# Kernel tuning notes

Measured on AMD Instinct MI355X. Metric: run time of the kernel, lower is better.

The kernel has to match this reference:

```python
import jax, jax.numpy as jnp
import numpy as np

B, SQ, SK = 2, 2048, 2048   # batch, n_query, n_memory
D, H, DFF = 1024, 16, 1024  # model dim, heads, ffn dim (must equal D per source constraints)
DH = D // H                 # head dim = 64
NEG = 1e9


def _split_heads(x):
    # (B, S, D) -> (B, H, S, DH)
    b, s, _ = x.shape
    return x.reshape(b, s, H, DH).transpose(0, 2, 1, 3)


def setup_inputs() -> dict:
    key = jax.random.key(0)
    ks = jax.random.split(key, 10)
    s = 0.02
    return {
        "q": jax.random.normal(ks[0], (B, SQ, D), jnp.float32),
        "k": jax.random.normal(ks[1], (B, SK, D), jnp.float32),
        "v": jax.random.normal(ks[2], (B, SK, D), jnp.float32),
        "Win_w": jax.random.normal(ks[3], (DFF, D), jnp.float32) * s,
        "Win_b": jnp.zeros((DFF,), jnp.float32),
        "Wff_w": jax.random.normal(ks[4], (D, DFF), jnp.float32) * s,
        "Wff_b": jnp.zeros((D,), jnp.float32),
        "Wout_w": jax.random.normal(ks[5], (D, D), jnp.float32) * s,
        "Wout_b": jnp.zeros((D,), jnp.float32),
        "attn_mask": jax.random.randint(ks[6], (B, SK), 0, 2, jnp.int32),
    }


def reference(q, k, v, Win_w, Win_b, Wff_w, Wff_b, Wout_w, Wout_b, attn_mask):
    # projections (in_linear; k,v additionally pass through out_linear as in source)
    qh = q @ Win_w.T + Win_b
    kh = (k @ Win_w.T + Win_b) @ Wout_w.T + Wout_b
    vh = (v @ Win_w.T + Win_b) @ Wout_w.T + Wout_b
    qh = qh * (D ** -0.5)

    qh, kh, vh = _split_heads(qh), _split_heads(kh), _split_heads(vh)

    # additive mask bias: 0 where mask==1, -1e9 where mask==0, broadcast over heads/queries
    bias = (attn_mask.astype(jnp.float32) - 1.0) * NEG  # (B, SK)
    scores = jnp.einsum("bhqd,bhkd->bhqk", qh, kh) + bias[:, None, None, :]
    probs = jax.nn.softmax(scores, axis=-1)
    out = jnp.einsum("bhqk,bhkd->bhqd", probs, vh)

    # merge heads: (B, H, SQ, DH) -> (B, SQ, D)
    out = out.transpose(0, 2, 1, 3).reshape(B, SQ, D)

    out = out @ Wff_w.T + Wff_b
    out = out @ Wout_w.T + Wout_b
    return out
```

## Files before the change

### kernel.cpp

```cpp
#include <hip/hip_runtime.h>
#include <cstdint>
#include <cstddef>

using u16 = unsigned short;
using u32 = unsigned int;

typedef __attribute__((ext_vector_type(8))) short short8;
typedef __attribute__((ext_vector_type(4))) float f32x4;

#define MFMA16(a, b, c) __builtin_amdgcn_mfma_f32_16x16x32_bf16((a), (b), (c), 0, 0, 0)

#define QSCALE 0.0450842200f

__device__ __forceinline__ u16 f2bf(float f) {
  u32 u = __float_as_uint(f);
  return (u16)((u + 0x7FFFu + ((u >> 16) & 1u)) >> 16);
}

__device__ __forceinline__ u32 pack_bf16(float a, float b) {
  u32 r;
  asm("v_cvt_pk_bf16_f32 %0, %1, %2" : "=v"(r) : "v"(a), "v"(b));
  return r;
}

__device__ __forceinline__ void gload_lds16(const u16* g, u16* l) {
  __builtin_amdgcn_global_load_lds((const __attribute__((address_space(1))) void*)g,
                                   (__attribute__((address_space(3))) void*)l, 16, 0, 0);
}

__global__ __launch_bounds__(256) void cvt_qkv(const float* __restrict__ q,
                                               const float* __restrict__ k,
                                               const float* __restrict__ v,
                                               u16* __restrict__ X) {
  int i4 = blockIdx.x * 256 + threadIdx.x;
  const float* src = (i4 < 1048576) ? q : (i4 < 2097152) ? k : v;
  int loc = i4 & 1048575;
  float4 w = reinterpret_cast<const float4*>(src)[loc];
  u32 lo = (u32)f2bf(w.x) | ((u32)f2bf(w.y) << 16);
  u32 hi = (u32)f2bf(w.z) | ((u32)f2bf(w.w) << 16);
  reinterpret_cast<uint2*>(X)[i4] = make_uint2(lo, hi);
}

__global__ __launch_bounds__(256) void prep(const float* __restrict__ Wout_w,
                                            const float* __restrict__ Win_w,
                                            const float* __restrict__ Wff_w,
                                            const float* __restrict__ Win_b,
                                            u16* __restrict__ Woutb, u16* __restrict__ Winb,
                                            u16* __restrict__ WinT, u16* __restrict__ WffT,
                                            float* __restrict__ bias1f) {
  __shared__ float tile[64][68];
  const int t = threadIdx.x;
  const int bid = blockIdx.x;
  if (bid < 2048) {
    const float* src = bid < 1024 ? Wout_w : Win_w;
    u16* dst = bid < 1024 ? Woutb : Winb;
    const float sc = bid < 1024 ? 1.0f : QSCALE;
    int i = (bid & 1023) * 256 + t;
    float4 v = reinterpret_cast<const float4*>(src)[i];
    u32 lo = (u32)f2bf(v.x * sc) | ((u32)f2bf(v.y * sc) << 16);
    u32 hi = (u32)f2bf(v.z * sc) | ((u32)f2bf(v.w * sc) << 16);
    reinterpret_cast<uint2*>(dst)[i] = make_uint2(lo, hi);
  } else if (bid < 2560) {
    const float* in = bid < 2304 ? Win_w : Wff_w;
    u16* out = bid < 2304 ? WinT : WffT;
    const int tix = (bid - 2048) & 255;
    const int bx = (tix >> 4) * 64, by = (tix & 15) * 64;
    const int r = t >> 2, c16 = (t & 3) * 16;
#pragma unroll
    for (int i = 0; i < 4; ++i)
      *reinterpret_cast<float4*>(&tile[r][c16 + i * 4]) =
          *reinterpret_cast<const float4*>(&in[(size_t)(bx + r) * 1024 + by + c16 + i * 4]);
    __syncthreads();
    const int jj = t >> 2, i16 = (t & 3) * 16;
#pragma unroll
    for (int i = 0; i < 4; ++i) {
      uint2 p;
      p.x = (u32)f2bf(tile[i16 + i * 4 + 0][jj]) | ((u32)f2bf(tile[i16 + i * 4 + 1][jj]) << 16);
      p.y = (u32)f2bf(tile[i16 + i * 4 + 2][jj]) | ((u32)f2bf(tile[i16 + i * 4 + 3][jj]) << 16);
      *reinterpret_cast<uint2*>(&out[(size_t)(by + jj) * 1024 + bx + i16 + i * 4]) = p;
    }
  } else {
    float4 v = reinterpret_cast<const float4*>(Win_b)[t];
    v.x *= QSCALE; v.y *= QSCALE; v.z *= QSCALE; v.w *= QSCALE;
    reinterpret_cast<float4*>(bias1f)[t] = v;
  }
}

__global__ __launch_bounds__(256) void bias_comb(const float* __restrict__ W,
                                                 const float* __restrict__ bin,
                                                 const float* __restrict__ badd,
                                                 float* __restrict__ outb) {
  const int w = threadIdx.x >> 6, l = threadIdx.x & 63;
  const int j = blockIdx.x * 4 + w;
  const float4* Wr = reinterpret_cast<const float4*>(W + (size_t)j * 1024);
  const float4* br = reinterpret_cast<const float4*>(bin);
  float s = 0.f;
  for (int i = l; i < 256; i += 64) {
    float4 a = Wr[i], b = br[i];
    s += a.x * b.x + a.y * b.y + a.z * b.z + a.w * b.w;
  }
#pragma unroll
  for (int o = 1; o < 64; o <<= 1) s += __shfl_xor(s, o);
  if (l == 0) outb[j] = s + badd[j];
}

__global__ __launch_bounds__(256) void gemm_w2(const u16* __restrict__ A,
                                               const u16* __restrict__ Bt0,
                                               const u16* __restrict__ Bt1,
                                               u16* __restrict__ C0,
                                               u16* __restrict__ C1) {
  const u16* Bt = blockIdx.z ? Bt1 : Bt0;
  u16* C = blockIdx.z ? C1 : C0;
  __shared__ __align__(16) u16 As[2][4096];
  __shared__ __align__(16) u16 Bs[2][4096];
  const int t = threadIdx.x, w = t >> 6, l = t & 63;
  const int l15 = l & 15, l4 = l >> 4;
  const int m0 = blockIdx.x * 64, n0 = blockIdx.y * 64;
  f32x4 acc[4] = {};
  const int row0 = t >> 3, cs0 = t & 7;
  const int c0 = cs0 ^ (row0 & 7);
  const int row1 = row0 + 32;
  const int c1 = cs0 ^ (row1 & 7);
  const u16* gA0 = A + (size_t)(m0 + row0) * 1024 + c0 * 8;
  const u16* gA1 = A + (size_t)(m0 + row1) * 1024 + c1 * 8;
  const u16* gB0 = Bt + (size_t)(n0 + row0) * 1024 + c0 * 8;
  const u16* gB1 = Bt + (size_t)(n0 + row1) * 1024 + c1 * 8;
#define W2_STAGE(KK, DST)                             \
  gload_lds16(gA0 + (KK), &As[DST][0] + w * 512);     \
  gload_lds16(gA1 + (KK), &As[DST][2048] + w * 512);  \
  gload_lds16(gB0 + (KK), &Bs[DST][0] + w * 512);     \
  gload_lds16(gB1 + (KK), &Bs[DST][2048] + w * 512);
  W2_STAGE(0, 0)
  for (int step = 0; step < 16; ++step) {
    const int c = step & 1;
    __syncthreads();
    if (step < 15) { W2_STAGE((step + 1) * 64, c ^ 1) }
#pragma unroll
    for (int ks = 0; ks < 2; ++ks) {
      const int cc = ks * 4 + l4;
      short8 bfr = *reinterpret_cast<const short8*>(&Bs[c][(w * 16 + l15) * 64 + ((cc ^ (l15 & 7)) * 8)]);
#pragma unroll
      for (int i = 0; i < 4; ++i) {
        short8 afr = *reinterpret_cast<const short8*>(&As[c][(i * 16 + l15) * 64 + ((cc ^ (l15 & 7)) * 8)]);
        acc[i] = MFMA16(afr, bfr, acc[i]);
      }
    }
  }
#pragma unroll
  for (int i = 0; i < 4; ++i)
#pragma unroll
    for (int j = 0; j < 4; ++j)
      C[(size_t)(m0 + i * 16 + l4 * 4 + j) * 1024 + n0 + w * 16 + l15] = f2bf(acc[i][j]);
}

__global__ __launch_bounds__(256) void proj(const u16* __restrict__ X,
                                            const u16* __restrict__ Winb,
                                            const u16* __restrict__ Wc2,
                                            const float* __restrict__ bias1f,
                                            const float* __restrict__ bias2,
                                            u16* __restrict__ Qh,
                                            u16* __restrict__ Kp,
                                            u16* __restrict__ VT) {
  __shared__ __align__(16) u16 As[2][4096];
  __shared__ __align__(16) u16 Bs[2][4096];
  const int t = threadIdx.x, w = t >> 6, l = t & 63;
  const int l15 = l & 15, l4 = l >> 4;
  const int seg = blockIdx.x >> 5;
  const int m0 = blockIdx.x * 128;
  const int n0 = blockIdx.y * 128;
  const int wr = (w >> 1) * 64, wc = (w & 1) * 64;
  const u16* Bt = seg == 0 ? Winb : Wc2;
  const float* bias = seg == 0 ? bias1f : bias2;

  f32x4 acc[4][4] = {};
  const u16* gA = X + (size_t)(m0 + (t >> 2)) * 1024 + (t & 3) * 8;
  const u16* gB = Bt + (size_t)(n0 + (t >> 2)) * 1024 + (t & 3) * 8;
#define PJ_STAGE(KK, DST)                                   \
  gload_lds16(gA + (KK), &As[DST][0] + w * 512);            \
  gload_lds16(gA + (KK) + 65536, &As[DST][2048] + w * 512); \
  gload_lds16(gB + (KK), &Bs[DST][0] + w * 512);            \
  gload_lds16(gB + (KK) + 65536, &Bs[DST][2048] + w * 512);
  PJ_STAGE(0, 0)
  for (int step = 0; step < 32; ++step) {
    const int c = step & 1;
    __syncthreads();
    if (step < 31) { PJ_STAGE((step + 1) * 32, c ^ 1) }
    short8 af[4], bf[4];
#pragma unroll
    for (int i = 0; i < 4; ++i)
      af[i] = *reinterpret_cast<const short8*>(&As[c][(wr + i * 16 + l15) * 32 + l4 * 8]);
#pragma unroll
    for (int i = 0; i < 4; ++i)
      bf[i] = *reinterpret_cast<const short8*>(&Bs[c][(wc + i * 16 + l15) * 32 + l4 * 8]);
#pragma unroll
    for (int mi = 0; mi < 4; ++mi)
#pragma unroll
      for (int ni = 0; ni < 4; ++ni)
        acc[mi][ni] = MFMA16(af[mi], bf[ni], acc[mi][ni]);
  }

#pragma unroll
  for (int mi = 0; mi < 4; ++mi) {
#pragma unroll
    for (int ni = 0; ni < 4; ++ni) {
      const int col = n0 + wc + ni * 16 + l15;
      const float bv = bias[col];
      const int row0 = m0 + wr + mi * 16 + l4 * 4;
      if (seg == 0) {
#pragma unroll
        for (int j = 0; j < 4; ++j)
          Qh[(size_t)(row0 + j) * 1024 + col] = f2bf(acc[mi][ni][j] + bv);
      } else if (seg == 1) {
#pragma unroll
        for (int j = 0; j < 4; ++j)
          Kp[(size_t)(row0 - 4096 + j) * 1024 + col] = f2bf(acc[mi][ni][j] + bv);
      } else {
        const int r = row0 - 8192;
        const int bb = r >> 11;
        const int sk = r & 2047;
        u32 p0 = (u32)f2bf(acc[mi][ni][0] + bv) | ((u32)f2bf(acc[mi][ni][1] + bv) << 16);
        u32 p1 = (u32)f2bf(acc[mi][ni][2] + bv) | ((u32)f2bf(acc[mi][ni][3] + bv) << 16);
        *reinterpret_cast<uint2*>(VT + ((size_t)(bb * 1024 + col)) * 2048 + sk) = make_uint2(p0, p1);
      }
    }
  }
}

__global__ __launch_bounds__(512) void attn(const u16* __restrict__ Qh,
                                            const u16* __restrict__ Kb,
                                            const u16* __restrict__ VT,
                                            const int* __restrict__ mask,
                                            u16* __restrict__ AO) {
  __shared__ __align__(16) u16 Kt[64 * 64];
  __shared__ __align__(16) u16 Vt[64 * 64];
  __shared__ __align__(16) u16 Pw[8 * 16 * 64];
  __shared__ float biasS[2048];
  const int t = threadIdx.x, l = t & 63, w = t >> 6;
  const int l15 = l & 15, l4 = l >> 4;
  const int q0 = blockIdx.x * 128;
  const int bh = blockIdx.y, b = bh >> 4, h = bh & 15;

  for (int i = t; i < 2048; i += 512) biasS[i] = mask[b * 2048 + i] ? 0.f : -1.442695e9f;

  short8 qf[2];
  {
    const u16* qp = Qh + (size_t)(b * 2048 + q0 + w * 16 + l15) * 1024 + h * 64 + l4 * 8;
    qf[0] = *reinterpret_cast<const short8*>(qp);
    qf[1] = *reinterpret_cast<const short8*>(qp + 32);
  }
  short8 ones;
#pragma unroll
  for (int i = 0; i < 8; ++i) ones[i] = (short)0x3F80;

  f32x4 acc[4] = {};
  f32x4 accS = {};

  const int rr = t >> 3, cs = t & 7;
  const int ck = cs ^ (rr & 7);
  const u16* gK = Kb + (size_t)(b * 2048 + rr) * 1024 + h * 64 + ck * 8;
  u16* ldsK = Kt + w * 512;
  const u32* gV = reinterpret_cast<const u32*>(VT) + (size_t)(b * 1024 + h * 64 + rr) * 1024 + ck;
  const int pws = w * 1024;

  for (int kt = 0; kt < 2048; kt += 64) {
    const u32* gvt = gV + (kt >> 1);
    u32 A0 = gvt[0], A1 = gvt[8], A2 = gvt[16], A3 = gvt[24];
    __syncthreads();
    gload_lds16(gK + (size_t)kt * 1024, ldsK);
    uint4 vv;
    vv.x = (A0 & 0xffffu) | (A1 << 16);
    vv.y = (A2 & 0xffffu) | (A3 << 16);
    vv.z = (A0 >> 16) | (A1 & 0xffff0000u);
    vv.w = (A2 >> 16) | (A3 & 0xffff0000u);
    *reinterpret_cast<uint4*>(&Vt[rr * 64 + cs * 8]) = vv;
    __syncthreads();

    f32x4 s[4] = {};
#pragma unroll
    for (int ks = 0; ks < 2; ++ks) {
      const int cc = ks * 4 + l4;
#pragma unroll
      for (int n = 0; n < 4; ++n) {
        short8 kb = *reinterpret_cast<const short8*>(&Kt[(n * 16 + l15) * 64 + ((cc ^ (l15 & 7)) * 8)]);
        s[n] = MFMA16(qf[ks], kb, s[n]);
      }
    }
#pragma unroll
    for (int n = 0; n < 4; ++n) {
      const float bv = biasS[kt + n * 16 + l15];
#pragma unroll
      for (int j = 0; j < 4; ++j) s[n][j] = __builtin_amdgcn_exp2f(s[n][j] + bv);
    }
#pragma unroll
    for (int j = 0; j < 4; ++j) {
      const int r = l4 * 4 + j;
      uint2 pk;
      pk.x = pack_bf16(s[0][j], s[1][j]);
      pk.y = pack_bf16(s[2][j], s[3][j]);
      *reinterpret_cast<uint2*>(
          &Pw[pws + r * 64 + (((l15 >> 1) ^ (r & 7)) * 8) + (l15 & 1) * 4]) = pk;
    }
#pragma unroll
    for (int ks = 0; ks < 2; ++ks) {
      const int cc = ks * 4 + l4;
      short8 pa = *reinterpret_cast<const short8*>(&Pw[pws + l15 * 64 + ((cc ^ (l15 & 7)) * 8)]);
#pragma unroll
      for (int n = 0; n < 4; ++n) {
        short8 vb = *reinterpret_cast<const short8*>(&Vt[(n * 16 + l15) * 64 + ((cc ^ (l15 & 7)) * 8)]);
        acc[n] = MFMA16(pa, vb, acc[n]);
      }
      accS = MFMA16(pa, ones, accS);
    }
  }

  const size_t orow0 = (size_t)(b * 2048 + q0 + w * 16 + l4 * 4);
#pragma unroll
  for (int j = 0; j < 4; ++j) {
    const float inv = 1.0f / accS[j];
#pragma unroll
    for (int n = 0; n < 4; ++n)
      AO[(orow0 + j) * 1024 + h * 64 + n * 16 + l15] = f2bf(acc[n][j] * inv);
  }
}

__global__ __launch_bounds__(256) void gemm_tail(const u16* __restrict__ A,
                                                 const u16* __restrict__ Bt,
                                                 const float* __restrict__ bias,
                                                 float* __restrict__ C) {
  __shared__ __align__(16) u16 As[2][4096];
  __shared__ __align__(16) u16 Bs[2][2048];
  const int t = threadIdx.x, w = t >> 6, l = t & 63;
  const int l15 = l & 15, l4 = l >> 4;
  const int m0 = blockIdx.x * 128, n0 = blockIdx.y * 64;
  const int wr = (w >> 1) * 64, wc = (w & 1) * 32;
  f32x4 acc[4][2] = {};
  const u16* gA = A + (size_t)(m0 + (t >> 2)) * 1024 + (t & 3) * 8;
  const u16* gB = Bt + (size_t)(n0 + (t >> 2)) * 1024 + (t & 3) * 8;
#define TL_STAGE(KK, DST)                                   \
  gload_lds16(gA + (KK), &As[DST][0] + w * 512);            \
  gload_lds16(gA + (KK) + 65536, &As[DST][2048] + w * 512); \
  gload_lds16(gB + (KK), &Bs[DST][0] + w * 512);
  TL_STAGE(0, 0)
  for (int step = 0; step < 32; ++step) {
    const int c = step & 1;
    __syncthreads();
    if (step < 31) { TL_STAGE((step + 1) * 32, c ^ 1) }
    short8 af[4], bf[2];
#pragma unroll
    for (int i = 0; i < 4; ++i)
      af[i] = *reinterpret_cast<const short8*>(&As[c][(wr + i * 16 + l15) * 32 + l4 * 8]);
#pragma unroll
    for (int i = 0; i < 2; ++i)
      bf[i] = *reinterpret_cast<const short8*>(&Bs[c][(wc + i * 16 + l15) * 32 + l4 * 8]);
#pragma unroll
    for (int mi = 0; mi < 4; ++mi)
#pragma unroll
      for (int ni = 0; ni < 2; ++ni)
        acc[mi][ni] = MFMA16(af[mi], bf[ni], acc[mi][ni]);
  }
#pragma unroll
  for (int mi = 0; mi < 4; ++mi) {
#pragma unroll
    for (int ni = 0; ni < 2; ++ni) {
      const int col = n0 + wc + ni * 16 + l15;
      const float bv = bias[col];
      const int row0 = m0 + wr + mi * 16 + l4 * 4;
#pragma unroll
      for (int j = 0; j < 4; ++j)
        C[(size_t)(row0 + j) * 1024 + col] = acc[mi][ni][j] + bv;
    }
  }
}

extern "C" void kernel_launch(void* const* d_in, const int* in_sizes, int n_in,
                              void* d_out, int out_size, void* d_ws, size_t ws_size,
                              hipStream_t stream) {
  const float* q = (const float*)d_in[0];
  const float* k = (const float*)d_in[1];
  const float* v = (const float*)d_in[2];
  const float* Win_w = (const float*)d_in[3];
  const float* Win_b = (const float*)d_in[4];
  const float* Wff_w = (const float*)d_in[5];
  const float* Wff_b = (const float*)d_in[6];
  const float* Wout_w = (const float*)d_in[7];
  const float* Wout_b = (const float*)d_in[8];
  const int* mask = (const int*)d_in[9];
  float* out = (float*)d_out;

  char* ws = (char*)d_ws;
  u16* Xbf = (u16*)ws;
  u16* AO = (u16*)ws;
  float* bias3 = (float*)(ws + 20971520);
  u16* Qh = (u16*)(ws + 25165824);
  u16* WinT = (u16*)(ws + 25165824);
  u16* Woutb = (u16*)(ws + 27262976);
  u16* WffT = (u16*)(ws + 29360128);
  u16* Kproj = (u16*)(ws + 33554432);
  u16* VT = (u16*)(ws + 41943040);
  u16* Wc2 = (u16*)(ws + 50331648);
  u16* Wc3 = (u16*)(ws + 52428800);
  u16* Winb = (u16*)(ws + 54525952);
  float* bias2 = out;
  float* bias1f = out + 1024;

  prep<<<2561, 256, 0, stream>>>(Wout_w, Win_w, Wff_w, Win_b, Woutb, Winb, WinT, WffT, bias1f);
  cvt_qkv<<<12288, 256, 0, stream>>>(q, k, v, Xbf);
  bias_comb<<<256, 256, 0, stream>>>(Wout_w, Win_b, Wout_b, bias2);
  gemm_w2<<<dim3(16, 16, 2), 256, 0, stream>>>(Woutb, WinT, WffT, Wc2, Wc3);
  proj<<<dim3(96, 8), 256, 0, stream>>>(Xbf, Winb, Wc2, bias1f, bias2, Qh, Kproj, VT);
  bias_comb<<<256, 256, 0, stream>>>(Wout_w, Wff_b, Wout_b, bias3);
  attn<<<dim3(16, 32), 512, 0, stream>>>(Qh, Kproj, VT, mask, AO);
  gemm_tail<<<dim3(32, 16), 256, 0, stream>>>(AO, Wc3, bias3, out);
}
```

Baseline: 160.3 us.

## Merge prep kernels into one launch and remap blocks for XCD-local L2 reuse

Folds cvt_qkv, prep and the first bias_comb into a single prep_all launch, which removes two kernel launches and their gaps. It also changes the GEMM and attention kernels to 1D grids with a block-index swizzle, so that blocks on the same XCD (round-robin by blockIdx & 7) work on nearby M tiles or the same batch/head and share L2 cache lines. The risks are a less balanced tile order and the added index arithmetic.

```diff
diff --git a/kernel.cpp b/kernel.cpp
--- a/kernel.cpp
+++ b/kernel.cpp
@@ -28,42 +28,40 @@
                                    (__attribute__((address_space(3))) void*)l, 16, 0, 0);
 }
 
-__global__ __launch_bounds__(256) void cvt_qkv(const float* __restrict__ q,
-                                               const float* __restrict__ k,
-                                               const float* __restrict__ v,
-                                               u16* __restrict__ X) {
-  int i4 = blockIdx.x * 256 + threadIdx.x;
-  const float* src = (i4 < 1048576) ? q : (i4 < 2097152) ? k : v;
-  int loc = i4 & 1048575;
-  float4 w = reinterpret_cast<const float4*>(src)[loc];
-  u32 lo = (u32)f2bf(w.x) | ((u32)f2bf(w.y) << 16);
-  u32 hi = (u32)f2bf(w.z) | ((u32)f2bf(w.w) << 16);
-  reinterpret_cast<uint2*>(X)[i4] = make_uint2(lo, hi);
-}
-
-__global__ __launch_bounds__(256) void prep(const float* __restrict__ Wout_w,
-                                            const float* __restrict__ Win_w,
-                                            const float* __restrict__ Wff_w,
-                                            const float* __restrict__ Win_b,
-                                            u16* __restrict__ Woutb, u16* __restrict__ Winb,
-                                            u16* __restrict__ WinT, u16* __restrict__ WffT,
-                                            float* __restrict__ bias1f) {
+__global__ __launch_bounds__(256) void prep_all(
+    const float* __restrict__ q, const float* __restrict__ k, const float* __restrict__ v,
+    const float* __restrict__ Wout_w, const float* __restrict__ Win_w,
+    const float* __restrict__ Wff_w, const float* __restrict__ Win_b,
+    const float* __restrict__ Wout_b, u16* __restrict__ X,
+    u16* __restrict__ Woutb, u16* __restrict__ Winb,
+    u16* __restrict__ WinT, u16* __restrict__ WffT,
+    float* __restrict__ bias2, float* __restrict__ bias1f) {
   __shared__ float tile[64][68];
   const int t = threadIdx.x;
   const int bid = blockIdx.x;
-  if (bid < 2048) {
-    const float* src = bid < 1024 ? Wout_w : Win_w;
-    u16* dst = bid < 1024 ? Woutb : Winb;
-    const float sc = bid < 1024 ? 1.0f : QSCALE;
-    int i = (bid & 1023) * 256 + t;
-    float4 v = reinterpret_cast<const float4*>(src)[i];
-    u32 lo = (u32)f2bf(v.x * sc) | ((u32)f2bf(v.y * sc) << 16);
-    u32 hi = (u32)f2bf(v.z * sc) | ((u32)f2bf(v.w * sc) << 16);
+  if (bid < 12288) {
+    int i4 = bid * 256 + t;
+    const float* src = (i4 < 1048576) ? q : (i4 < 2097152) ? k : v;
+    int loc = i4 & 1048575;
+    float4 w = reinterpret_cast<const float4*>(src)[loc];
+    u32 lo = (u32)f2bf(w.x) | ((u32)f2bf(w.y) << 16);
+    u32 hi = (u32)f2bf(w.z) | ((u32)f2bf(w.w) << 16);
+    reinterpret_cast<uint2*>(X)[i4] = make_uint2(lo, hi);
+  } else if (bid < 14336) {
+    const int wb = bid - 12288;
+    const float* src = wb < 1024 ? Wout_w : Win_w;
+    u16* dst = wb < 1024 ? Woutb : Winb;
+    const float sc = wb < 1024 ? 1.0f : QSCALE;
+    int i = (wb & 1023) * 256 + t;
+    float4 vv = reinterpret_cast<const float4*>(src)[i];
+    u32 lo = (u32)f2bf(vv.x * sc) | ((u32)f2bf(vv.y * sc) << 16);
+    u32 hi = (u32)f2bf(vv.z * sc) | ((u32)f2bf(vv.w * sc) << 16);
     reinterpret_cast<uint2*>(dst)[i] = make_uint2(lo, hi);
-  } else if (bid < 2560) {
-    const float* in = bid < 2304 ? Win_w : Wff_w;
-    u16* out = bid < 2304 ? WinT : WffT;
-    const int tix = (bid - 2048) & 255;
+  } else if (bid < 14848) {
+    const int tb = bid - 14336;
+    const float* in = tb < 256 ? Win_w : Wff_w;
+    u16* out = tb < 256 ? WinT : WffT;
+    const int tix = tb & 255;
     const int bx = (tix >> 4) * 64, by = (tix & 15) * 64;
     const int r = t >> 2, c16 = (t & 3) * 16;
 #pragma unroll
@@ -79,10 +77,23 @@
       p.y = (u32)f2bf(tile[i16 + i * 4 + 2][jj]) | ((u32)f2bf(tile[i16 + i * 4 + 3][jj]) << 16);
       *reinterpret_cast<uint2*>(&out[(size_t)(by + jj) * 1024 + bx + i16 + i * 4]) = p;
     }
+  } else if (bid < 15104) {
+    const int w = t >> 6, l = t & 63;
+    const int j = (bid - 14848) * 4 + w;
+    const float4* Wr = reinterpret_cast<const float4*>(Wout_w + (size_t)j * 1024);
+    const float4* br = reinterpret_cast<const float4*>(Win_b);
+    float s = 0.f;
+    for (int i = l; i < 256; i += 64) {
+      float4 a = Wr[i], b = br[i];
+      s += a.x * b.x + a.y * b.y + a.z * b.z + a.w * b.w;
+    }
+#pragma unroll
+    for (int o = 1; o < 64; o <<= 1) s += __shfl_xor(s, o);
+    if (l == 0) bias2[j] = s + Wout_b[j];
   } else {
-    float4 v = reinterpret_cast<const float4*>(Win_b)[t];
-    v.x *= QSCALE; v.y *= QSCALE; v.z *= QSCALE; v.w *= QSCALE;
-    reinterpret_cast<float4*>(bias1f)[t] = v;
+    float4 vv = reinterpret_cast<const float4*>(Win_b)[t];
+    vv.x *= QSCALE; vv.y *= QSCALE; vv.z *= QSCALE; vv.w *= QSCALE;
+    reinterpret_cast<float4*>(bias1f)[t] = vv;
   }
 }
 
@@ -109,13 +120,18 @@
                                                const u16* __restrict__ Bt1,
                                                u16* __restrict__ C0,
                                                u16* __restrict__ C1) {
-  const u16* Bt = blockIdx.z ? Bt1 : Bt0;
-  u16* C = blockIdx.z ? C1 : C0;
+  const int bid = blockIdx.x;
+  const int xcd = bid & 7, local = bid >> 3;
+  const int z = local >> 5;
+  const int mt = xcd * 2 + ((local >> 4) & 1);
+  const int nt = local & 15;
+  const u16* Bt = z ? Bt1 : Bt0;
+  u16* C = z ? C1 : C0;
   __shared__ __align__(16) u16 As[2][4096];
   __shared__ __align__(16) u16 Bs[2][4096];
   const int t = threadIdx.x, w = t >> 6, l = t & 63;
   const int l15 = l & 15, l4 = l >> 4;
-  const int m0 = blockIdx.x * 64, n0 = blockIdx.y * 64;
+  const int m0 = mt * 64, n0 = nt * 64;
   f32x4 acc[4] = {};
   const int row0 = t >> 3, cs0 = t & 7;
   const int c0 = cs0 ^ (row0 & 7);
@@ -165,9 +181,13 @@
   __shared__ __align__(16) u16 Bs[2][4096];
   const int t = threadIdx.x, w = t >> 6, l = t & 63;
   const int l15 = l & 15, l4 = l >> 4;
-  const int seg = blockIdx.x >> 5;
-  const int m0 = blockIdx.x * 128;
-  const int n0 = blockIdx.y * 128;
+  const int bid = blockIdx.x;
+  const int xcd = bid & 7, local = bid >> 3;
+  const int mt = xcd * 12 + (local >> 3);
+  const int nt = local & 7;
+  const int seg = mt >> 5;
+  const int m0 = mt * 128;
+  const int n0 = nt * 128;
   const int wr = (w >> 1) * 64, wc = (w & 1) * 64;
   const u16* Bt = seg == 0 ? Winb : Wc2;
   const float* bias = seg == 0 ? bias1f : bias2;
@@ -237,8 +257,10 @@
   __shared__ float biasS[2048];
   const int t = threadIdx.x, l = t & 63, w = t >> 6;
   const int l15 = l & 15, l4 = l >> 4;
-  const int q0 = blockIdx.x * 128;
-  const int bh = blockIdx.y, b = bh >> 4, h = bh & 15;
+  const int bid = blockIdx.x;
+  const int bh = (bid & 7) * 4 + ((bid >> 3) & 3);
+  const int qb = bid >> 5;
+  const int b = bh >> 4, h = bh & 15, q0 = qb * 128;
 
   for (int i = t; i < 2048; i += 512) biasS[i] = mask[b * 2048 + i] ? 0.f : -1.442695e9f;
 
@@ -331,7 +353,11 @@
   __shared__ __align__(16) u16 Bs[2][2048];
   const int t = threadIdx.x, w = t >> 6, l = t & 63;
   const int l15 = l & 15, l4 = l >> 4;
-  const int m0 = blockIdx.x * 128, n0 = blockIdx.y * 64;
+  const int bid = blockIdx.x;
+  const int xcd = bid & 7, local = bid >> 3;
+  const int mt = xcd * 4 + (local >> 4);
+  const int nt = local & 15;
+  const int m0 = mt * 128, n0 = nt * 64;
   const int wr = (w >> 1) * 64, wc = (w & 1) * 32;
   f32x4 acc[4][2] = {};
   const u16* gA = A + (size_t)(m0 + (t >> 2)) * 1024 + (t & 3) * 8;
@@ -403,12 +429,11 @@
   float* bias2 = out;
   float* bias1f = out + 1024;
 
-  prep<<<2561, 256, 0, stream>>>(Wout_w, Win_w, Wff_w, Win_b, Woutb, Winb, WinT, WffT, bias1f);
-  cvt_qkv<<<12288, 256, 0, stream>>>(q, k, v, Xbf);
-  bias_comb<<<256, 256, 0, stream>>>(Wout_w, Win_b, Wout_b, bias2);
-  gemm_w2<<<dim3(16, 16, 2), 256, 0, stream>>>(Woutb, WinT, WffT, Wc2, Wc3);
-  proj<<<dim3(96, 8), 256, 0, stream>>>(Xbf, Winb, Wc2, bias1f, bias2, Qh, Kproj, VT);
+  prep_all<<<15105, 256, 0, stream>>>(q, k, v, Wout_w, Win_w, Wff_w, Win_b, Wout_b,
+                                      Xbf, Woutb, Winb, WinT, WffT, bias2, bias1f);
+  gemm_w2<<<512, 256, 0, stream>>>(Woutb, WinT, WffT, Wc2, Wc3);
+  proj<<<768, 256, 0, stream>>>(Xbf, Winb, Wc2, bias1f, bias2, Qh, Kproj, VT);
   bias_comb<<<256, 256, 0, stream>>>(Wout_w, Wff_b, Wout_b, bias3);
-  attn<<<dim3(16, 32), 512, 0, stream>>>(Qh, Kproj, VT, mask, AO);
-  gemm_tail<<<dim3(32, 16), 256, 0, stream>>>(AO, Wc3, bias3, out);
-}
+  attn<<<512, 512, 0, stream>>>(Qh, Kproj, VT, mask, AO);
+  gemm_tail<<<512, 256, 0, stream>>>(AO, Wc3, bias3, out);
+}
```

New measurement: 151.2 us. 5.7% less time.
